# Performance work log

Measured on AMD Instinct MI355X. Metric: run time of the kernel, lower is better.

The kernel has to match this reference:

```python
import jax, jax.numpy as jnp
import numpy as np

N = 1_000_000   # total points across batch
INC = 128       # channel width (inc)
B = 16          # number of scans in batch
HID = INC // 4  # reduction=4


def setup_inputs() -> dict:
    key = jax.random.key(0)
    k1, k2, k3, k4 = jax.random.split(key, 4)
    feats = jax.random.normal(k1, (N, INC), dtype=jnp.float32)
    batch_idx = jnp.sort(jax.random.randint(k2, (N,), 0, B, dtype=jnp.int32))
    W1 = jax.random.normal(k3, (INC, HID), dtype=jnp.float32) * 0.05
    b1 = jnp.zeros((HID,), dtype=jnp.float32)
    W2 = jax.random.normal(k4, (HID, INC), dtype=jnp.float32) * 0.05
    b2 = jnp.zeros((INC,), dtype=jnp.float32)
    return {"feats": feats, "batch_idx": batch_idx, "W1": W1, "b1": b1, "W2": W2, "b2": b2}


def reference(feats, batch_idx, W1, b1, W2, b2):
    # Segment (per-scan) mean and max over points -> [B, INC].
    counts = jax.ops.segment_sum(jnp.ones((feats.shape[0],), feats.dtype), batch_idx, num_segments=B)
    seg_sum = jax.ops.segment_sum(feats, batch_idx, num_segments=B)
    seg_mean = seg_sum / jnp.maximum(counts, 1.0)[:, None]
    seg_max = jax.ops.segment_max(feats, batch_idx, num_segments=B)
    seg_max = jnp.where(counts[:, None] > 0, seg_max, 0.0)  # guard empty segments

    def mlp(z):
        return jax.nn.relu(z @ W1 + b1) @ W2 + b2

    # sigmoid(MLP(avg) + MLP(max)); pooled values are identical for every
    # point of a segment, so apply MLP on [B, INC] and gather per point.
    gate = jax.nn.sigmoid(mlp(seg_mean) + mlp(seg_max))  # [B, INC]
    return feats * gate[batch_idx]                        # [N, INC]
```

## Files before the change

### kernel.cpp

```cpp
#include <hip/hip_runtime.h>
#include <math.h>

#define INC   128
#define HID   32
#define NSEG  16

__device__ __forceinline__ unsigned f2ord(float f) {
    unsigned u = __float_as_uint(f);
    return (u & 0x80000000u) ? ~u : (u | 0x80000000u);
}
__device__ __forceinline__ float ord2f(unsigned u) {
    return (u & 0x80000000u) ? __uint_as_float(u & 0x7fffffffu)
                             : __uint_as_float(~u);
}

__device__ __forceinline__ void flush_lds(int seg, int c4, const float4& sm,
                                          const float4& mx, float cnt,
                                          float* s_sum, unsigned* s_max, float* s_cnt) {
    int base = seg * INC + c4 * 4;
    atomicAdd(&s_sum[base + 0], sm.x);
    atomicAdd(&s_sum[base + 1], sm.y);
    atomicAdd(&s_sum[base + 2], sm.z);
    atomicAdd(&s_sum[base + 3], sm.w);
    atomicMax(&s_max[base + 0], f2ord(mx.x));
    atomicMax(&s_max[base + 1], f2ord(mx.y));
    atomicMax(&s_max[base + 2], f2ord(mx.z));
    atomicMax(&s_max[base + 3], f2ord(mx.w));
    if (c4 == 0) atomicAdd(&s_cnt[seg], cnt);
}

__global__ __launch_bounds__(256) void seg_reduce_kernel(
    const float4* __restrict__ feats4, const int* __restrict__ bidx,
    float* __restrict__ gsum, unsigned* __restrict__ gmax,
    float* __restrict__ gcnt, int nrows)
{
    __shared__ float    s_sum[NSEG * INC];
    __shared__ unsigned s_max[NSEG * INC];
    __shared__ float    s_cnt[NSEG];

    const int tid   = threadIdx.x;
    const int chunk = (nrows + gridDim.x - 1) / gridDim.x;
    const int start = blockIdx.x * chunk;
    if (start >= nrows) return;
    const int end = min(start + chunk, nrows);

    for (int i = tid; i < NSEG * INC; i += 256) { s_sum[i] = 0.f; s_max[i] = 0u; }
    if (tid < NSEG) s_cnt[tid] = 0.f;
    __syncthreads();

    const int c4   = tid & 31;
    const int slot = tid >> 5;
    int    cur = -1;
    float4 sm  = make_float4(0.f, 0.f, 0.f, 0.f);
    float4 mx  = make_float4(0.f, 0.f, 0.f, 0.f);
    float  cnt = 0.f;

    for (int r = start + slot; r < end; r += 8) {
        int    seg = bidx[r];
        float4 f   = feats4[(size_t)r * (INC / 4) + c4];
        if (seg != cur) {
            if (cur >= 0) flush_lds(cur, c4, sm, mx, cnt, s_sum, s_max, s_cnt);
            cur = seg; sm = f; mx = f; cnt = 1.f;
        } else {
            sm.x += f.x; sm.y += f.y; sm.z += f.z; sm.w += f.w;
            mx.x = fmaxf(mx.x, f.x); mx.y = fmaxf(mx.y, f.y);
            mx.z = fmaxf(mx.z, f.z); mx.w = fmaxf(mx.w, f.w);
            cnt += 1.f;
        }
    }
    if (cur >= 0) flush_lds(cur, c4, sm, mx, cnt, s_sum, s_max, s_cnt);
    __syncthreads();

    const int sf = bidx[start];
    const int sl = bidx[end - 1];
    for (int s = sf; s <= sl; s++) {
        if (tid < INC) {
            atomicAdd(&gsum[s * INC + tid], s_sum[s * INC + tid]);
            atomicMax(&gmax[s * INC + tid], s_max[s * INC + tid]);
        }
        if (tid == 0) atomicAdd(&gcnt[s], s_cnt[s]);
    }
}

__global__ __launch_bounds__(256) void mlp_kernel(
    const float* __restrict__ gsum, const unsigned* __restrict__ gmax,
    const float* __restrict__ gcnt,
    const float* __restrict__ W1, const float* __restrict__ b1,
    const float* __restrict__ W2, const float* __restrict__ b2,
    float* __restrict__ gate)
{
    __shared__ float s_mean[NSEG * INC];
    __shared__ float s_max [NSEG * INC];
    __shared__ float s_h   [NSEG * HID];
    const int tid = threadIdx.x;

    for (int i = tid; i < NSEG * INC; i += 256) {
        int   s = i >> 7;
        float c = gcnt[s];
        s_mean[i] = gsum[i] / fmaxf(c, 1.f);
        s_max[i]  = (c > 0.f) ? ord2f(gmax[i]) : 0.f;
    }
    __syncthreads();

    for (int i = tid; i < NSEG * HID; i += 256) {
        int s = i / HID, h = i % HID;
        float am = b1[h], ax = b1[h];
        for (int c = 0; c < INC; c++) {
            float w = W1[c * HID + h];
            am += s_mean[s * INC + c] * w;
            ax += s_max [s * INC + c] * w;
        }
        s_h[i] = fmaxf(am, 0.f) + fmaxf(ax, 0.f);
    }
    __syncthreads();

    for (int i = tid; i < NSEG * INC; i += 256) {
        int s = i >> 7, c = i & (INC - 1);
        float a = 2.f * b2[c];
        for (int h = 0; h < HID; h++) a += s_h[s * HID + h] * W2[h * INC + c];
        gate[i] = 1.f / (1.f + expf(-a));
    }
}

__global__ __launch_bounds__(256) void apply_kernel(
    const float4* __restrict__ feats4, const int* __restrict__ bidx,
    const float4* __restrict__ gate4, float4* __restrict__ out4, int nrows)
{
    __shared__ float4 s_gate[NSEG * (INC / 4)];
    for (int i = threadIdx.x; i < NSEG * (INC / 4); i += blockDim.x)
        s_gate[i] = gate4[i];
    __syncthreads();

    const int total = nrows * (INC / 4);
    for (int idx = blockIdx.x * blockDim.x + threadIdx.x; idx < total;
         idx += gridDim.x * blockDim.x) {
        int    r   = idx >> 5;
        int    c4  = idx & 31;
        int    seg = bidx[r];
        float4 f   = feats4[idx];
        float4 g   = s_gate[seg * (INC / 4) + c4];
        out4[idx]  = make_float4(f.x * g.x, f.y * g.y, f.z * g.z, f.w * g.w);
    }
}

extern "C" void kernel_launch(void* const* d_in, const int* in_sizes, int n_in,
                              void* d_out, int out_size, void* d_ws, size_t ws_size,
                              hipStream_t stream) {
    const float* feats = (const float*)d_in[0];
    const int*   bidx  = (const int*)d_in[1];
    const float* W1    = (const float*)d_in[2];
    const float* b1    = (const float*)d_in[3];
    const float* W2    = (const float*)d_in[4];
    const float* b2    = (const float*)d_in[5];
    float*       out   = (float*)d_out;
    const int nrows    = in_sizes[1];

    char*     ws   = (char*)d_ws;
    float*    gsum = (float*)(ws);
    unsigned* gmax = (unsigned*)(ws + 8192);
    float*    gcnt = (float*)(ws + 16384);
    float*    gate = (float*)(ws + 16448);

    hipMemsetAsync(d_ws, 0, 16448, stream);

    seg_reduce_kernel<<<2048, 256, 0, stream>>>(
        (const float4*)feats, bidx, gsum, gmax, gcnt, nrows);
    mlp_kernel<<<1, 256, 0, stream>>>(gsum, gmax, gcnt, W1, b1, W2, b2, gate);
    apply_kernel<<<8192, 256, 0, stream>>>(
        (const float4*)feats, bidx, (const float4*)gate, (float4*)out, nrows);
}
```

Measured before the change: 966.9 us.

## Use nontemporal loads/stores, 8-wide reduce per thread, and stage MLP weights in LDS

New measurement: 926.5 us. 4.2% less time.

```diff
diff --git a/kernel.cpp b/kernel.cpp
--- a/kernel.cpp
+++ b/kernel.cpp
@@ -5,6 +5,17 @@
 #define HID   32
 #define NSEG  16
 
+typedef float f4v __attribute__((ext_vector_type(4)));
+
+__device__ __forceinline__ float4 ntload4(const float4* p) {
+    f4v v = __builtin_nontemporal_load((const f4v*)p);
+    return make_float4(v.x, v.y, v.z, v.w);
+}
+__device__ __forceinline__ void ntstore4(float4* p, float4 f) {
+    f4v v = {f.x, f.y, f.z, f.w};
+    __builtin_nontemporal_store(v, (f4v*)p);
+}
+
 __device__ __forceinline__ unsigned f2ord(float f) {
     unsigned u = __float_as_uint(f);
     return (u & 0x80000000u) ? ~u : (u | 0x80000000u);
@@ -14,19 +25,29 @@
                              : __uint_as_float(~u);
 }
 
-__device__ __forceinline__ void flush_lds(int seg, int c4, const float4& sm,
-                                          const float4& mx, float cnt,
-                                          float* s_sum, unsigned* s_max, float* s_cnt) {
-    int base = seg * INC + c4 * 4;
-    atomicAdd(&s_sum[base + 0], sm.x);
-    atomicAdd(&s_sum[base + 1], sm.y);
-    atomicAdd(&s_sum[base + 2], sm.z);
-    atomicAdd(&s_sum[base + 3], sm.w);
-    atomicMax(&s_max[base + 0], f2ord(mx.x));
-    atomicMax(&s_max[base + 1], f2ord(mx.y));
-    atomicMax(&s_max[base + 2], f2ord(mx.z));
-    atomicMax(&s_max[base + 3], f2ord(mx.w));
-    if (c4 == 0) atomicAdd(&s_cnt[seg], cnt);
+__device__ __forceinline__ void flush_lds8(int seg, int c8,
+                                           const float4& s0, const float4& s1,
+                                           const float4& m0, const float4& m1,
+                                           float cnt, float* s_sum,
+                                           unsigned* s_max, float* s_cnt) {
+    int base = seg * INC + c8 * 8;
+    atomicAdd(&s_sum[base + 0], s0.x);
+    atomicAdd(&s_sum[base + 1], s0.y);
+    atomicAdd(&s_sum[base + 2], s0.z);
+    atomicAdd(&s_sum[base + 3], s0.w);
+    atomicAdd(&s_sum[base + 4], s1.x);
+    atomicAdd(&s_sum[base + 5], s1.y);
+    atomicAdd(&s_sum[base + 6], s1.z);
+    atomicAdd(&s_sum[base + 7], s1.w);
+    atomicMax(&s_max[base + 0], f2ord(m0.x));
+    atomicMax(&s_max[base + 1], f2ord(m0.y));
+    atomicMax(&s_max[base + 2], f2ord(m0.z));
+    atomicMax(&s_max[base + 3], f2ord(m0.w));
+    atomicMax(&s_max[base + 4], f2ord(m1.x));
+    atomicMax(&s_max[base + 5], f2ord(m1.y));
+    atomicMax(&s_max[base + 6], f2ord(m1.z));
+    atomicMax(&s_max[base + 7], f2ord(m1.w));
+    if (c8 == 0) atomicAdd(&s_cnt[seg], cnt);
 }
 
 __global__ __launch_bounds__(256) void seg_reduce_kernel(
@@ -48,37 +69,41 @@
     if (tid < NSEG) s_cnt[tid] = 0.f;
     __syncthreads();
 
-    const int c4   = tid & 31;
-    const int slot = tid >> 5;
+    const int c8   = tid & 15;
+    const int slot = tid >> 4;
     int    cur = -1;
-    float4 sm  = make_float4(0.f, 0.f, 0.f, 0.f);
-    float4 mx  = make_float4(0.f, 0.f, 0.f, 0.f);
+    float4 s0 = make_float4(0.f, 0.f, 0.f, 0.f), s1 = s0;
+    float4 m0 = s0, m1 = s0;
     float  cnt = 0.f;
 
-    for (int r = start + slot; r < end; r += 8) {
-        int    seg = bidx[r];
-        float4 f   = feats4[(size_t)r * (INC / 4) + c4];
+    for (int r = start + slot; r < end; r += 16) {
+        int           seg  = bidx[r];
+        const float4* rowp = feats4 + (size_t)r * (INC / 4) + c8 * 2;
+        float4        f0   = ntload4(rowp);
+        float4        f1   = ntload4(rowp + 1);
         if (seg != cur) {
-            if (cur >= 0) flush_lds(cur, c4, sm, mx, cnt, s_sum, s_max, s_cnt);
-            cur = seg; sm = f; mx = f; cnt = 1.f;
+            if (cur >= 0) flush_lds8(cur, c8, s0, s1, m0, m1, cnt, s_sum, s_max, s_cnt);
+            cur = seg; s0 = f0; s1 = f1; m0 = f0; m1 = f1; cnt = 1.f;
         } else {
-            sm.x += f.x; sm.y += f.y; sm.z += f.z; sm.w += f.w;
-            mx.x = fmaxf(mx.x, f.x); mx.y = fmaxf(mx.y, f.y);
-            mx.z = fmaxf(mx.z, f.z); mx.w = fmaxf(mx.w, f.w);
+            s0.x += f0.x; s0.y += f0.y; s0.z += f0.z; s0.w += f0.w;
+            s1.x += f1.x; s1.y += f1.y; s1.z += f1.z; s1.w += f1.w;
+            m0.x = fmaxf(m0.x, f0.x); m0.y = fmaxf(m0.y, f0.y);
+            m0.z = fmaxf(m0.z, f0.z); m0.w = fmaxf(m0.w, f0.w);
+            m1.x = fmaxf(m1.x, f1.x); m1.y = fmaxf(m1.y, f1.y);
+            m1.z = fmaxf(m1.z, f1.z); m1.w = fmaxf(m1.w, f1.w);
             cnt += 1.f;
         }
     }
-    if (cur >= 0) flush_lds(cur, c4, sm, mx, cnt, s_sum, s_max, s_cnt);
-    __syncthreads();
-
-    const int sf = bidx[start];
-    const int sl = bidx[end - 1];
-    for (int s = sf; s <= sl; s++) {
-        if (tid < INC) {
-            atomicAdd(&gsum[s * INC + tid], s_sum[s * INC + tid]);
-            atomicMax(&gmax[s * INC + tid], s_max[s * INC + tid]);
-        }
-        if (tid == 0) atomicAdd(&gcnt[s], s_cnt[s]);
+    if (cur >= 0) flush_lds8(cur, c8, s0, s1, m0, m1, cnt, s_sum, s_max, s_cnt);
+    __syncthreads();
+
+    const int sf  = bidx[start];
+    const int sl  = bidx[end - 1];
+    const int col = tid & (INC - 1);
+    for (int s = sf + (tid >> 7); s <= sl; s += 2) {
+        atomicAdd(&gsum[s * INC + col], s_sum[s * INC + col]);
+        atomicMax(&gmax[s * INC + col], s_max[s * INC + col]);
+        if (col == 0) atomicAdd(&gcnt[s], s_cnt[s]);
     }
 }
 
@@ -92,7 +117,15 @@
     __shared__ float s_mean[NSEG * INC];
     __shared__ float s_max [NSEG * INC];
     __shared__ float s_h   [NSEG * HID];
+    __shared__ float s_W1  [INC * HID];
+    __shared__ float s_W2  [HID * INC];
+    __shared__ float s_b1  [HID];
+    __shared__ float s_b2  [INC];
     const int tid = threadIdx.x;
+
+    for (int i = tid; i < INC * HID; i += 256) { s_W1[i] = W1[i]; s_W2[i] = W2[i]; }
+    if (tid < HID) s_b1[tid] = b1[tid];
+    if (tid < INC) s_b2[tid] = b2[tid];
 
     for (int i = tid; i < NSEG * INC; i += 256) {
         int   s = i >> 7;
@@ -104,9 +137,9 @@
 
     for (int i = tid; i < NSEG * HID; i += 256) {
         int s = i / HID, h = i % HID;
-        float am = b1[h], ax = b1[h];
+        float am = s_b1[h], ax = s_b1[h];
         for (int c = 0; c < INC; c++) {
-            float w = W1[c * HID + h];
+            float w = s_W1[c * HID + h];
             am += s_mean[s * INC + c] * w;
             ax += s_max [s * INC + c] * w;
         }
@@ -116,8 +149,8 @@
 
     for (int i = tid; i < NSEG * INC; i += 256) {
         int s = i >> 7, c = i & (INC - 1);
-        float a = 2.f * b2[c];
-        for (int h = 0; h < HID; h++) a += s_h[s * HID + h] * W2[h * INC + c];
+        float a = 2.f * s_b2[c];
+        for (int h = 0; h < HID; h++) a += s_h[s * HID + h] * s_W2[h * INC + c];
         gate[i] = 1.f / (1.f + expf(-a));
     }
 }
@@ -137,9 +170,10 @@
         int    r   = idx >> 5;
         int    c4  = idx & 31;
         int    seg = bidx[r];
-        float4 f   = feats4[idx];
+        float4 f   = ntload4(&feats4[idx]);
         float4 g   = s_gate[seg * (INC / 4) + c4];
-        out4[idx]  = make_float4(f.x * g.x, f.y * g.y, f.z * g.z, f.w * g.w);
+        ntstore4(&out4[idx],
+                 make_float4(f.x * g.x, f.y * g.y, f.z * g.z, f.w * g.w));
     }
 }
 
```
